# Optimization experiments

Hardware: AMD Instinct MI355X
Metric: run time of the kernel (lower is better)

The kernel has to match this reference:

```python
import jax, jax.numpy as jnp
import numpy as np

EPSILON = 0.0

def setup_inputs() -> dict:
    key = jax.random.key(0)
    k1, k2, k3, k4, k5 = jax.random.split(key, 5)
    N, MAX_NB, D_IN, D_OUT, N_BONDS = 50000, 16, 256, 256, 400000
    x = jax.random.normal(k1, (N, D_IN), dtype=jnp.float32)
    W = jax.random.normal(k2, (D_OUT, D_IN), dtype=jnp.float32) * (1.0 / np.sqrt(D_IN))
    b = jax.random.normal(k3, (D_OUT,), dtype=jnp.float32) * 0.01
    b_from_a = jax.random.randint(k4, (N_BONDS,), 0, N, dtype=jnp.int32)
    a_from_b = jax.random.randint(k5, (N, MAX_NB), 0, N_BONDS, dtype=jnp.int32)
    return {"x": x, "W": W, "b": b, "b_from_a": b_from_a, "a_from_b": a_from_b}

def reference(x, W, b, b_from_a, a_from_b):
    # a2a[i, k] = source atom of the k-th neighbor bond of atom i
    a2a = b_from_a[a_from_b]                      # [N, max_nb]
    h = x @ W.T + b                               # [N, d_out]
    h = h.at[0].set(0.0)                          # row 0 is padding
    message = h[a2a]                              # [N, max_nb, d_out] gather
    out = (1.0 + EPSILON) * h + jnp.sum(message, axis=1)
    return jax.nn.relu(out)
```

## Files before the change

### kernel.cpp

```cpp
#include <hip/hip_runtime.h>

typedef short bf16x8 __attribute__((ext_vector_type(8)));
typedef float f32x4  __attribute__((ext_vector_type(4)));

__device__ __forceinline__ unsigned short f32_to_bf16(float f) {
  union { float f; unsigned int u; } v; v.f = f;
  unsigned int u = v.u;
  u += 0x7fffu + ((u >> 16) & 1u);
  return (unsigned short)(u >> 16);
}
__device__ __forceinline__ float bf16lo_to_f32(unsigned int u) {
  union { unsigned int u; float f; } v; v.u = u << 16; return v.f;
}
__device__ __forceinline__ float bf16hi_to_f32(unsigned int u) {
  union { unsigned int u; float f; } v; v.u = u & 0xffff0000u; return v.f;
}

__global__ __launch_bounds__(256, 2) void gin_gemm(
    const float* __restrict__ x, const float* __restrict__ W,
    const float* __restrict__ bias, unsigned short* __restrict__ h, int M) {
  __shared__ __align__(16) unsigned short As[64 * 32];
  __shared__ __align__(16) unsigned short Bs[256 * 32];

  const int tid  = threadIdx.x;
  const int wid  = tid >> 6;
  const int lane = tid & 63;
  const int row0 = blockIdx.x * 64;

  f32x4 acc[4][4] = {};

  const int srow = tid >> 2;
  const int sk0  = (tid & 3) << 3;
  int agrow = row0 + srow;
  if (agrow >= M) agrow = M - 1;
  const float* aRow = x + (size_t)agrow * 256 + sk0;
  const float* bRow = W + (size_t)srow * 256 + sk0;

  for (int kt = 0; kt < 8; ++kt) {
    const int kb = kt * 32;
    {
      float4 v0 = *(const float4*)(aRow + kb);
      float4 v1 = *(const float4*)(aRow + kb + 4);
      bf16x8 u;
      u[0] = (short)f32_to_bf16(v0.x); u[1] = (short)f32_to_bf16(v0.y);
      u[2] = (short)f32_to_bf16(v0.z); u[3] = (short)f32_to_bf16(v0.w);
      u[4] = (short)f32_to_bf16(v1.x); u[5] = (short)f32_to_bf16(v1.y);
      u[6] = (short)f32_to_bf16(v1.z); u[7] = (short)f32_to_bf16(v1.w);
      *(bf16x8*)(&As[srow * 32 + sk0]) = u;
    }
#pragma unroll
    for (int j = 0; j < 4; ++j) {
      const float* p = bRow + (size_t)(j * 64) * 256 + kb;
      float4 v0 = *(const float4*)p;
      float4 v1 = *(const float4*)(p + 4);
      bf16x8 u;
      u[0] = (short)f32_to_bf16(v0.x); u[1] = (short)f32_to_bf16(v0.y);
      u[2] = (short)f32_to_bf16(v0.z); u[3] = (short)f32_to_bf16(v0.w);
      u[4] = (short)f32_to_bf16(v1.x); u[5] = (short)f32_to_bf16(v1.y);
      u[6] = (short)f32_to_bf16(v1.z); u[7] = (short)f32_to_bf16(v1.w);
      *(bf16x8*)(&Bs[(j * 64 + srow) * 32 + sk0]) = u;
    }
    __syncthreads();

    const int r16 = lane & 15;
    const int qk  = (lane >> 4) << 3;
    bf16x8 af[4], bfr[4];
#pragma unroll
    for (int g = 0; g < 4; ++g)
      af[g] = *(const bf16x8*)(&As[(g * 16 + r16) * 32 + qk]);
#pragma unroll
    for (int g = 0; g < 4; ++g)
      bfr[g] = *(const bf16x8*)(&Bs[(wid * 64 + g * 16 + r16) * 32 + qk]);
#pragma unroll
    for (int rg = 0; rg < 4; ++rg)
#pragma unroll
      for (int cg = 0; cg < 4; ++cg)
        acc[rg][cg] = __builtin_amdgcn_mfma_f32_16x16x32_bf16(
            af[rg], bfr[cg], acc[rg][cg], 0, 0, 0);
    __syncthreads();
  }

  const int quad = lane >> 4;
  const int c16  = lane & 15;
#pragma unroll
  for (int rg = 0; rg < 4; ++rg) {
#pragma unroll
    for (int r = 0; r < 4; ++r) {
      int grow = row0 + rg * 16 + quad * 4 + r;
      if (grow >= M) continue;
#pragma unroll
      for (int cg = 0; cg < 4; ++cg) {
        int col = wid * 64 + cg * 16 + c16;
        float v = acc[rg][cg][r] + bias[col];
        if (grow == 0) v = 0.0f;
        h[(size_t)grow * 256 + col] = f32_to_bf16(v);
      }
    }
  }
}

__global__ __launch_bounds__(256, 4) void gin_gather(
    const unsigned short* __restrict__ h, const int* __restrict__ b_from_a,
    const int* __restrict__ a_from_b, float* __restrict__ out, int N) {
  const int tid  = threadIdx.x;
  const int wid  = tid >> 6;
  const int lane = tid & 63;
  const int half = lane >> 5;
  const int l32  = lane & 31;
  const int i0   = blockIdx.x * 8 + wid * 2;
  if (i0 >= N) return;
  const int row  = i0 + half;
  const int rowc = (row < N) ? row : (N - 1);

  int src = 0;
  if (lane < 32) {
    int idx = i0 * 16 + lane;
    int lim = N * 16 - 1;
    if (idx > lim) idx = lim;
    src = b_from_a[a_from_b[idx]];
  }

  const int c0 = l32 * 8;
  uint4 u = *(const uint4*)(h + (size_t)rowc * 256 + c0);
  float a0 = bf16lo_to_f32(u.x), a1 = bf16hi_to_f32(u.x);
  float a2 = bf16lo_to_f32(u.y), a3 = bf16hi_to_f32(u.y);
  float a4 = bf16lo_to_f32(u.z), a5 = bf16hi_to_f32(u.z);
  float a6 = bf16lo_to_f32(u.w), a7 = bf16hi_to_f32(u.w);

#pragma unroll
  for (int k = 0; k < 16; ++k) {
    int s = __shfl(src, half * 16 + k, 64);
    uint4 v = *(const uint4*)(h + (size_t)s * 256 + c0);
    a0 += bf16lo_to_f32(v.x); a1 += bf16hi_to_f32(v.x);
    a2 += bf16lo_to_f32(v.y); a3 += bf16hi_to_f32(v.y);
    a4 += bf16lo_to_f32(v.z); a5 += bf16hi_to_f32(v.z);
    a6 += bf16lo_to_f32(v.w); a7 += bf16hi_to_f32(v.w);
  }

  if (row < N) {
    f32x4 r0, r1;
    r0[0] = fmaxf(a0, 0.0f); r0[1] = fmaxf(a1, 0.0f);
    r0[2] = fmaxf(a2, 0.0f); r0[3] = fmaxf(a3, 0.0f);
    r1[0] = fmaxf(a4, 0.0f); r1[1] = fmaxf(a5, 0.0f);
    r1[2] = fmaxf(a6, 0.0f); r1[3] = fmaxf(a7, 0.0f);
    float* op = out + (size_t)row * 256 + c0;
    __builtin_nontemporal_store(r0, (f32x4*)op);
    __builtin_nontemporal_store(r1, (f32x4*)(op + 4));
  }
}

extern "C" void kernel_launch(void* const* d_in, const int* in_sizes, int n_in,
                              void* d_out, int out_size, void* d_ws, size_t ws_size,
                              hipStream_t stream) {
  const float* x        = (const float*)d_in[0];
  const float* W        = (const float*)d_in[1];
  const float* b        = (const float*)d_in[2];
  const int*   b_from_a = (const int*)d_in[3];
  const int*   a_from_b = (const int*)d_in[4];
  float*       out      = (float*)d_out;
  const int M = in_sizes[0] / 256;

  unsigned short* h = (unsigned short*)d_ws;

  gin_gemm<<<(M + 63) / 64, 256, 0, stream>>>(x, W, b, h, M);
  gin_gather<<<(M + 7) / 8, 256, 0, stream>>>(h, b_from_a, a_from_b, out, M);
}
```

Before: 191.0 us.

## Store h in column-sliced layout and gather per slice for cache locality

The GEMM can now write h as 8 column slices of 32 bf16 each, so each slice (M*64 bytes, about 3.2MB) fits in L2/MALL while the gather kernel works through one slice at a time. The a2a index composition moves into its own precompute kernel. The new gather uses grid-stride blocks interleaved across slices, with 4 lanes per atom. The cost is an extra kernel launch, extra workspace for a2a, and scattered 2-byte stores in the GEMM epilogue. The path runs only when the workspace is large enough.

```diff
diff --git a/kernel.cpp b/kernel.cpp
--- a/kernel.cpp
+++ b/kernel.cpp
@@ -2,6 +2,8 @@
 
 typedef short bf16x8 __attribute__((ext_vector_type(8)));
 typedef float f32x4  __attribute__((ext_vector_type(4)));
+typedef int   i32x4  __attribute__((ext_vector_type(4)));
+typedef unsigned int u32x4 __attribute__((ext_vector_type(4)));
 
 __device__ __forceinline__ unsigned short f32_to_bf16(float f) {
   union { float f; unsigned int u; } v; v.f = f;
@@ -18,7 +20,8 @@
 
 __global__ __launch_bounds__(256, 2) void gin_gemm(
     const float* __restrict__ x, const float* __restrict__ W,
-    const float* __restrict__ bias, unsigned short* __restrict__ h, int M) {
+    const float* __restrict__ bias, unsigned short* __restrict__ h, int M,
+    int sliced) {
   __shared__ __align__(16) unsigned short As[64 * 32];
   __shared__ __align__(16) unsigned short Bs[256 * 32];
 
@@ -93,8 +96,79 @@
         int col = wid * 64 + cg * 16 + c16;
         float v = acc[rg][cg][r] + bias[col];
         if (grow == 0) v = 0.0f;
-        h[(size_t)grow * 256 + col] = f32_to_bf16(v);
+        unsigned short hv = f32_to_bf16(v);
+        if (sliced) {
+          h[((size_t)(col >> 5) * M + grow) * 32 + (col & 31)] = hv;
+        } else {
+          h[(size_t)grow * 256 + col] = hv;
+        }
       }
+    }
+  }
+}
+
+__global__ __launch_bounds__(256, 8) void gin_a2a(
+    const int* __restrict__ b_from_a, const int* __restrict__ a_from_b,
+    int* __restrict__ a2a, int n) {
+  int j = (blockIdx.x * 256 + threadIdx.x) * 4;
+  if (j + 3 >= n) {
+    for (; j < n; ++j) a2a[j] = b_from_a[a_from_b[j]];
+    return;
+  }
+  i32x4 f = *(const i32x4*)(a_from_b + j);
+  i32x4 r;
+  r[0] = b_from_a[f[0]]; r[1] = b_from_a[f[1]];
+  r[2] = b_from_a[f[2]]; r[3] = b_from_a[f[3]];
+  *(i32x4*)(a2a + j) = r;
+}
+
+__global__ __launch_bounds__(256, 8) void gin_gather_sliced(
+    const unsigned short* __restrict__ hs, const int* __restrict__ a2a,
+    float* __restrict__ out, int M) {
+  const int tid   = threadIdx.x;
+  const int wid   = tid >> 6;
+  const int lane  = tid & 63;
+  const int slice = blockIdx.x & 7;
+  const int chunk = blockIdx.x >> 3;
+  const int a     = lane >> 2;
+  const int sub   = lane & 3;
+  const unsigned short* __restrict__ hsl = hs + (size_t)slice * M * 32;
+  const int ngroups = (M + 15) >> 4;
+
+  for (int g = chunk * 4 + wid; g < ngroups; g += 1024) {
+    const int i0 = g * 16;
+    int idx = i0 * 16 + lane * 4;
+    int lim = M * 16 - 4;
+    if (idx > lim) idx = lim;
+    i32x4 ids = __builtin_nontemporal_load((const i32x4*)(a2a + idx));
+
+    float s0 = 0, s1 = 0, s2 = 0, s3 = 0, s4 = 0, s5 = 0, s6 = 0, s7 = 0;
+#pragma unroll
+    for (int k = 0; k < 16; ++k) {
+      int id = __shfl(ids[k & 3], a * 4 + (k >> 2), 64);
+      u32x4 v = *(const u32x4*)(hsl + (size_t)id * 32 + sub * 8);
+      s0 += bf16lo_to_f32(v[0]); s1 += bf16hi_to_f32(v[0]);
+      s2 += bf16lo_to_f32(v[1]); s3 += bf16hi_to_f32(v[1]);
+      s4 += bf16lo_to_f32(v[2]); s5 += bf16hi_to_f32(v[2]);
+      s6 += bf16lo_to_f32(v[3]); s7 += bf16hi_to_f32(v[3]);
+    }
+    const int self  = i0 + a;
+    const int selfc = self < M ? self : M - 1;
+    u32x4 v = *(const u32x4*)(hsl + (size_t)selfc * 32 + sub * 8);
+    s0 += bf16lo_to_f32(v[0]); s1 += bf16hi_to_f32(v[0]);
+    s2 += bf16lo_to_f32(v[1]); s3 += bf16hi_to_f32(v[1]);
+    s4 += bf16lo_to_f32(v[2]); s5 += bf16hi_to_f32(v[2]);
+    s6 += bf16lo_to_f32(v[3]); s7 += bf16hi_to_f32(v[3]);
+
+    if (self < M) {
+      f32x4 r0, r1;
+      r0[0] = fmaxf(s0, 0.0f); r0[1] = fmaxf(s1, 0.0f);
+      r0[2] = fmaxf(s2, 0.0f); r0[3] = fmaxf(s3, 0.0f);
+      r1[0] = fmaxf(s4, 0.0f); r1[1] = fmaxf(s5, 0.0f);
+      r1[2] = fmaxf(s6, 0.0f); r1[3] = fmaxf(s7, 0.0f);
+      float* op = out + (size_t)self * 256 + slice * 32 + sub * 8;
+      __builtin_nontemporal_store(r0, (f32x4*)op);
+      __builtin_nontemporal_store(r1, (f32x4*)(op + 4));
     }
   }
 }
@@ -161,7 +235,17 @@
   const int M = in_sizes[0] / 256;
 
   unsigned short* h = (unsigned short*)d_ws;
-
-  gin_gemm<<<(M + 63) / 64, 256, 0, stream>>>(x, W, b, h, M);
-  gin_gather<<<(M + 7) / 8, 256, 0, stream>>>(h, b_from_a, a_from_b, out, M);
-}
+  const size_t h_bytes   = (size_t)M * 256 * sizeof(unsigned short);
+  const size_t a2a_bytes = (size_t)M * 16 * sizeof(int);
+
+  if (ws_size >= h_bytes + a2a_bytes) {
+    int* a2a = (int*)((char*)d_ws + h_bytes);
+    const int n = M * 16;
+    gin_a2a<<<(n / 4 + 255) / 256, 256, 0, stream>>>(b_from_a, a_from_b, a2a, n);
+    gin_gemm<<<(M + 63) / 64, 256, 0, stream>>>(x, W, b, h, M, 1);
+    gin_gather_sliced<<<2048, 256, 0, stream>>>(h, a2a, out, M);
+  } else {
+    gin_gemm<<<(M + 63) / 64, 256, 0, stream>>>(x, W, b, h, M, 0);
+    gin_gather<<<(M + 7) / 8, 256, 0, stream>>>(h, b_from_a, a_from_b, out, M);
+  }
+}
```

After: 312.0 us. +63.4%, slower.

## Load GEMM MFMA fragments directly from global memory, removing LDS staging

Applied to the files above, without the earlier changes.

The GEMM kernel no longer stages x and W tiles through shared memory with barriers. Each wave now loads its own A and B fragments straight from global memory, converts them to bf16 in registers, and feeds the MFMAs. This removes LDS writes and reads and both __syncthreads per k-step, and the occupancy hint is raised from 2 to 3 blocks. The cost is that all four waves redundantly load the same x rows, and fragment-shaped loads (32-byte chunks strided by row) coalesce worse, so global and L2 traffic goes up.

```diff
diff --git a/kernel.cpp b/kernel.cpp
--- a/kernel.cpp
+++ b/kernel.cpp
@@ -16,68 +16,58 @@
   union { unsigned int u; float f; } v; v.u = u & 0xffff0000u; return v.f;
 }
 
-__global__ __launch_bounds__(256, 2) void gin_gemm(
+__device__ __forceinline__ bf16x8 cvt_f32x8_bf16(float4 v0, float4 v1) {
+  bf16x8 u;
+  u[0] = (short)f32_to_bf16(v0.x); u[1] = (short)f32_to_bf16(v0.y);
+  u[2] = (short)f32_to_bf16(v0.z); u[3] = (short)f32_to_bf16(v0.w);
+  u[4] = (short)f32_to_bf16(v1.x); u[5] = (short)f32_to_bf16(v1.y);
+  u[6] = (short)f32_to_bf16(v1.z); u[7] = (short)f32_to_bf16(v1.w);
+  return u;
+}
+
+__global__ __launch_bounds__(256, 3) void gin_gemm(
     const float* __restrict__ x, const float* __restrict__ W,
     const float* __restrict__ bias, unsigned short* __restrict__ h, int M) {
-  __shared__ __align__(16) unsigned short As[64 * 32];
-  __shared__ __align__(16) unsigned short Bs[256 * 32];
-
   const int tid  = threadIdx.x;
   const int wid  = tid >> 6;
   const int lane = tid & 63;
   const int row0 = blockIdx.x * 64;
+  const int r16  = lane & 15;
+  const int qk   = (lane >> 4) << 3;
 
   f32x4 acc[4][4] = {};
 
-  const int srow = tid >> 2;
-  const int sk0  = (tid & 3) << 3;
-  int agrow = row0 + srow;
-  if (agrow >= M) agrow = M - 1;
-  const float* aRow = x + (size_t)agrow * 256 + sk0;
-  const float* bRow = W + (size_t)srow * 256 + sk0;
+  const float* aP[4];
+  const float* bP[4];
+#pragma unroll
+  for (int g = 0; g < 4; ++g) {
+    int ar = row0 + g * 16 + r16;
+    if (ar >= M) ar = M - 1;
+    aP[g] = x + (size_t)ar * 256 + qk;
+    bP[g] = W + (size_t)(wid * 64 + g * 16 + r16) * 256 + qk;
+  }
 
   for (int kt = 0; kt < 8; ++kt) {
     const int kb = kt * 32;
-    {
-      float4 v0 = *(const float4*)(aRow + kb);
-      float4 v1 = *(const float4*)(aRow + kb + 4);
-      bf16x8 u;
-      u[0] = (short)f32_to_bf16(v0.x); u[1] = (short)f32_to_bf16(v0.y);
-      u[2] = (short)f32_to_bf16(v0.z); u[3] = (short)f32_to_bf16(v0.w);
-      u[4] = (short)f32_to_bf16(v1.x); u[5] = (short)f32_to_bf16(v1.y);
-      u[6] = (short)f32_to_bf16(v1.z); u[7] = (short)f32_to_bf16(v1.w);
-      *(bf16x8*)(&As[srow * 32 + sk0]) = u;
+    bf16x8 af[4], bfr[4];
+#pragma unroll
+    for (int g = 0; g < 4; ++g) {
+      float4 v0 = *(const float4*)(aP[g] + kb);
+      float4 v1 = *(const float4*)(aP[g] + kb + 4);
+      af[g] = cvt_f32x8_bf16(v0, v1);
     }
 #pragma unroll
-    for (int j = 0; j < 4; ++j) {
-      const float* p = bRow + (size_t)(j * 64) * 256 + kb;
-      float4 v0 = *(const float4*)p;
-      float4 v1 = *(const float4*)(p + 4);
-      bf16x8 u;
-      u[0] = (short)f32_to_bf16(v0.x); u[1] = (short)f32_to_bf16(v0.y);
-      u[2] = (short)f32_to_bf16(v0.z); u[3] = (short)f32_to_bf16(v0.w);
-      u[4] = (short)f32_to_bf16(v1.x); u[5] = (short)f32_to_bf16(v1.y);
-      u[6] = (short)f32_to_bf16(v1.z); u[7] = (short)f32_to_bf16(v1.w);
-      *(bf16x8*)(&Bs[(j * 64 + srow) * 32 + sk0]) = u;
+    for (int g = 0; g < 4; ++g) {
+      float4 v0 = *(const float4*)(bP[g] + kb);
+      float4 v1 = *(const float4*)(bP[g] + kb + 4);
+      bfr[g] = cvt_f32x8_bf16(v0, v1);
     }
-    __syncthreads();
-
-    const int r16 = lane & 15;
-    const int qk  = (lane >> 4) << 3;
-    bf16x8 af[4], bfr[4];
-#pragma unroll
-    for (int g = 0; g < 4; ++g)
-      af[g] = *(const bf16x8*)(&As[(g * 16 + r16) * 32 + qk]);
-#pragma unroll
-    for (int g = 0; g < 4; ++g)
-      bfr[g] = *(const bf16x8*)(&Bs[(wid * 64 + g * 16 + r16) * 32 + qk]);
 #pragma unroll
     for (int rg = 0; rg < 4; ++rg)
 #pragma unroll
       for (int cg = 0; cg < 4; ++cg)
         acc[rg][cg] = __builtin_amdgcn_mfma_f32_16x16x32_bf16(
             af[rg], bfr[cg], acc[rg][cg], 0, 0, 0);
-    __syncthreads();
   }
 
   const int quad = lane >> 4;
```

After: 238.0 us. 1.25x slower.
